# Optimization experiments

Measured on AMD Instinct MI355X. Metric: run time of the kernel, lower is better.

Reference implementation:

```python
import jax, jax.numpy as jnp
import numpy as np

STATE_LEN, SEQ_LEN, HIDDEN = 2048, 4096, 2048

def setup_inputs() -> dict:
    key = jax.random.key(0)
    k1, k2, k3, k4 = jax.random.split(key, 4)
    scale = 1.0 / np.sqrt(HIDDEN)
    return {
        "out_state": jax.random.normal(k1, (STATE_LEN, HIDDEN), dtype=jnp.float32),
        "history": jax.random.normal(k2, (SEQ_LEN, HIDDEN), dtype=jnp.float32),
        "W": jax.random.normal(k3, (HIDDEN, HIDDEN), dtype=jnp.float32) * scale,
        "b": jax.random.normal(k4, (HIDDEN,), dtype=jnp.float32) * scale,
    }

def reference(out_state, history, W, b):
    # method='general': energy_j = Linear(history_j) = history_j @ W.T + b
    # score[i, j] = out_state_i . energy_j  -> batched GEMM replacing the double loop
    energies = history @ W.T + b                 # [seq_len, hidden]
    scores = jnp.einsum('ih,jh->ij', out_state, energies)  # [state_len, seq_len]
    # F.softmax on a 2D tensor (legacy default) normalizes over dim=1 (rows)
    return jax.nn.softmax(scores, axis=-1)
```

## Files before the change

kernel.cpp:

```cpp
#include <hip/hip_runtime.h>


#define STATE_LEN 2048
#define SEQ_LEN   4096
#define HIDDEN    2048

#define BM 128
#define BN 128
#define BK 32

#define WAIT_VM8   0x0F78
#define WAIT_VM0   0x0F70
#define WAIT_LGKM0 0xC07F

typedef __bf16 bf16x8 __attribute__((ext_vector_type(8)));
typedef float f32x4 __attribute__((ext_vector_type(4)));

__device__ __forceinline__ unsigned short f32_to_bf16(float f) {
  unsigned u = __float_as_uint(f);
  u += 0x7FFFu + ((u >> 16) & 1u);
  return (unsigned short)(u >> 16);
}
__device__ __forceinline__ float bf16_to_f32(unsigned short h) {
  return __uint_as_float(((unsigned)h) << 16);
}

__device__ __forceinline__ void gld16(const void* g, void* l) {
  __builtin_amdgcn_global_load_lds(
      (const __attribute__((address_space(1))) unsigned int*)g,
      (__attribute__((address_space(3))) unsigned int*)l,
      16, 0, 0);
}

__global__ __launch_bounds__(256) void pack_all(
    const float* __restrict__ os, const float* __restrict__ hist,
    const float* __restrict__ W,
    unsigned short* __restrict__ ohi, unsigned short* __restrict__ olo,
    unsigned short* __restrict__ hhi, unsigned short* __restrict__ hlo,
    unsigned short* __restrict__ wthi, unsigned short* __restrict__ wtlo) {
  const int bx = blockIdx.x;
  const int t = threadIdx.x;
  if (bx < 12288) {
    const float* in;
    unsigned short *hi, *lo;
    int i;
    if (bx < 4096) {
      in = os; hi = ohi; lo = olo; i = (bx * 256 + t) * 4;
    } else {
      in = hist; hi = hhi; lo = hlo; i = ((bx - 4096) * 256 + t) * 4;
    }
    float4 v = *(const float4*)&in[i];
    ushort4 h, l;
    h.x = f32_to_bf16(v.x); l.x = f32_to_bf16(v.x - bf16_to_f32(h.x));
    h.y = f32_to_bf16(v.y); l.y = f32_to_bf16(v.y - bf16_to_f32(h.y));
    h.z = f32_to_bf16(v.z); l.z = f32_to_bf16(v.z - bf16_to_f32(h.z));
    h.w = f32_to_bf16(v.w); l.w = f32_to_bf16(v.w - bf16_to_f32(h.w));
    *(ushort4*)&hi[i] = h;
    *(ushort4*)&lo[i] = l;
  } else {
    __shared__ float tile[64][65];
    const int bt = bx - 12288;
    const int h0 = (bt & 31) * 64;
    const int k0 = (bt >> 5) * 64;
    const int lr = t >> 4;
    const int c4 = (t & 15) * 4;
#pragma unroll
    for (int pass = 0; pass < 4; ++pass) {
      const int row = pass * 16 + lr;
      float4 v = *(const float4*)&W[(size_t)(h0 + row) * HIDDEN + k0 + c4];
      tile[row][c4] = v.x; tile[row][c4 + 1] = v.y;
      tile[row][c4 + 2] = v.z; tile[row][c4 + 3] = v.w;
    }
    __syncthreads();
#pragma unroll
    for (int pass = 0; pass < 4; ++pass) {
      const int kl = pass * 16 + (t >> 4);
      const int hl = (t & 15) * 4;
      ushort4 h4, l4;
#pragma unroll
      for (int j = 0; j < 4; ++j) {
        const float x = tile[hl + j][kl];
        const unsigned short h = f32_to_bf16(x);
        ((unsigned short*)&h4)[j] = h;
        ((unsigned short*)&l4)[j] = f32_to_bf16(x - bf16_to_f32(h));
      }
      const size_t o = (size_t)(k0 + kl) * HIDDEN + h0 + hl;
      *(ushort4*)&wthi[o] = h4;
      *(ushort4*)&wtlo[o] = l4;
    }
  }
}

__global__ __launch_bounds__(256) void reduce_split2(
    const float* __restrict__ p0, const float* __restrict__ p1,
    unsigned short* __restrict__ hi, unsigned short* __restrict__ lo, int n) {
  int i = (blockIdx.x * 256 + threadIdx.x) * 4;
  if (i >= n) return;
  float4 a = *(const float4*)&p0[i];
  float4 b = *(const float4*)&p1[i];
  a.x += b.x; a.y += b.y; a.z += b.z; a.w += b.w;
  ushort4 h, l;
  h.x = f32_to_bf16(a.x); l.x = f32_to_bf16(a.x - bf16_to_f32(h.x));
  h.y = f32_to_bf16(a.y); l.y = f32_to_bf16(a.y - bf16_to_f32(h.y));
  h.z = f32_to_bf16(a.z); l.z = f32_to_bf16(a.z - bf16_to_f32(h.z));
  h.w = f32_to_bf16(a.w); l.w = f32_to_bf16(a.w - bf16_to_f32(h.w));
  *(ushort4*)&hi[i] = h;
  *(ushort4*)&lo[i] = l;
}

template <int KSPLIT>
__global__ __launch_bounds__(256, 2) void gemm_pipe(
    const unsigned short* __restrict__ Ahi, const unsigned short* __restrict__ Alo,
    const unsigned short* __restrict__ Bhi, const unsigned short* __restrict__ Blo,
    float* __restrict__ Cf0, float* __restrict__ Cf1, int M, int N, int K) {
  __shared__ __align__(16) unsigned short sA[2][2][BM * BK];
  __shared__ __align__(16) unsigned short sB[2][2][BN * BK];

  const int t = threadIdx.x;
  const int tileM = blockIdx.y * BM;
  const int tileN = blockIdx.x * BN;
  const int z = (KSPLIT > 1) ? blockIdx.z : 0;
  const int kBase = z * (K / KSPLIT);
  const int iters = (K / KSPLIT) / BK;
  float* Cf = (KSPLIT > 1 && z == 1) ? Cf1 : Cf0;

  const int rr = t >> 2;
  const int cc = t & 3;

  const int lane = t & 63;
  const int wave = t >> 6;
  const int wm = wave >> 1;
  const int wn = wave & 1;
  const int lr = lane & 15;
  const int kqc = lane >> 4;

  f32x4 acc[4][4] = {};

  auto stage = [&](int buf, int k0) {
#pragma unroll
    for (int p = 0; p < 2; ++p) {
      const int r = p * 64 + rr;
      const int q = cc ^ ((r >> 1) & 3);
      const size_t ga = (size_t)(tileM + r) * K + k0 + q * 8;
      const size_t gb = (size_t)(tileN + r) * K + k0 + q * 8;
      const int ls = r * BK + cc * 8;
      gld16(Ahi + ga, &sA[buf][0][ls]);
      gld16(Alo + ga, &sA[buf][1][ls]);
      gld16(Bhi + gb, &sB[buf][0][ls]);
      gld16(Blo + gb, &sB[buf][1][ls]);
    }
  };

  stage(0, kBase);

  for (int it = 0; it < iters; ++it) {
    const int buf = it & 1;
    if (it + 1 < iters) {
      stage(buf ^ 1, kBase + (it + 1) * BK);
      __builtin_amdgcn_s_waitcnt(WAIT_VM8);
    } else {
      __builtin_amdgcn_s_waitcnt(WAIT_VM0);
    }
    __builtin_amdgcn_s_barrier();

    bf16x8 ah[4], al[4], bh[4], bl[4];
#pragma unroll
    for (int mi = 0; mi < 4; ++mi) {
      const int R = wm * 64 + mi * 16 + lr;
      const int off = R * BK + (kqc ^ ((R >> 1) & 3)) * 8;
      ah[mi] = *(const bf16x8*)&sA[buf][0][off];
      al[mi] = *(const bf16x8*)&sA[buf][1][off];
    }
#pragma unroll
    for (int ni = 0; ni < 4; ++ni) {
      const int R = wn * 64 + ni * 16 + lr;
      const int off = R * BK + (kqc ^ ((R >> 1) & 3)) * 8;
      bh[ni] = *(const bf16x8*)&sB[buf][0][off];
      bl[ni] = *(const bf16x8*)&sB[buf][1][off];
    }
#pragma unroll
    for (int mi = 0; mi < 4; ++mi)
#pragma unroll
      for (int ni = 0; ni < 4; ++ni) {
        acc[mi][ni] = __builtin_amdgcn_mfma_f32_16x16x32_bf16(ah[mi], bh[ni], acc[mi][ni], 0, 0, 0);
        acc[mi][ni] = __builtin_amdgcn_mfma_f32_16x16x32_bf16(ah[mi], bl[ni], acc[mi][ni], 0, 0, 0);
        acc[mi][ni] = __builtin_amdgcn_mfma_f32_16x16x32_bf16(al[mi], bh[ni], acc[mi][ni], 0, 0, 0);
      }

    __builtin_amdgcn_s_waitcnt(WAIT_LGKM0);
    __builtin_amdgcn_s_barrier();
  }

#pragma unroll
  for (int mi = 0; mi < 4; ++mi)
#pragma unroll
    for (int ni = 0; ni < 4; ++ni)
#pragma unroll
      for (int e = 0; e < 4; ++e) {
        const int row = tileM + wm * 64 + mi * 16 + (lane >> 4) * 4 + e;
        const int col = tileN + wn * 64 + ni * 16 + lr;
        Cf[(size_t)row * N + col] = acc[mi][ni][e];
      }
}

__global__ __launch_bounds__(256) void softmax_rows(float* __restrict__ d, int cols) {
  const int row = blockIdx.x;
  float* p = d + (size_t)row * cols;
  const int t = threadIdx.x;
  const int lane = t & 63;
  const int wave = t >> 6;
  __shared__ float sred[4];

  float4 v[4];
  float m = -3.0e38f;
#pragma unroll
  for (int k = 0; k < 4; ++k) {
    v[k] = *(float4*)&p[(t + k * 256) * 4];
    m = fmaxf(m, fmaxf(fmaxf(v[k].x, v[k].y), fmaxf(v[k].z, v[k].w)));
  }
#pragma unroll
  for (int off = 32; off > 0; off >>= 1) m = fmaxf(m, __shfl_xor(m, off, 64));
  if (lane == 0) sred[wave] = m;
  __syncthreads();
  m = fmaxf(fmaxf(sred[0], sred[1]), fmaxf(sred[2], sred[3]));
  __syncthreads();

  float s = 0.f;
#pragma unroll
  for (int k = 0; k < 4; ++k) {
    v[k].x = __expf(v[k].x - m);
    v[k].y = __expf(v[k].y - m);
    v[k].z = __expf(v[k].z - m);
    v[k].w = __expf(v[k].w - m);
    s += (v[k].x + v[k].y) + (v[k].z + v[k].w);
  }
#pragma unroll
  for (int off = 32; off > 0; off >>= 1) s += __shfl_xor(s, off, 64);
  if (lane == 0) sred[wave] = s;
  __syncthreads();
  s = (sred[0] + sred[1]) + (sred[2] + sred[3]);
  const float inv = 1.0f / s;
#pragma unroll
  for (int k = 0; k < 4; ++k) {
    v[k].x *= inv; v[k].y *= inv; v[k].z *= inv; v[k].w *= inv;
    *(float4*)&p[(t + k * 256) * 4] = v[k];
  }
}

extern "C" void kernel_launch(void* const* d_in, const int* in_sizes, int n_in,
                              void* d_out, int out_size, void* d_ws, size_t ws_size,
                              hipStream_t stream) {
  const float* out_state = (const float*)d_in[0];
  const float* history   = (const float*)d_in[1];
  const float* W         = (const float*)d_in[2];
  float* out = (float*)d_out;

  char* ws = (char*)d_ws;
  const size_t MB = 1ull << 20;
  unsigned short* ohi  = (unsigned short*)(ws + 0 * MB);
  unsigned short* olo  = (unsigned short*)(ws + 8 * MB);
  unsigned short* wthi = (unsigned short*)(ws + 16 * MB);
  unsigned short* wtlo = (unsigned short*)(ws + 24 * MB);
  unsigned short* hhi  = (unsigned short*)(ws + 32 * MB);
  unsigned short* hlo  = (unsigned short*)(ws + 48 * MB);
  float*          pws  = (float*)(ws + 64 * MB);
  float* g1p0 = pws;
  float* g1p1 = pws + (size_t)STATE_LEN * HIDDEN;
  unsigned short* thi = (unsigned short*)(ws + 0 * MB);
  unsigned short* tlo = (unsigned short*)(ws + 8 * MB);

  pack_all<<<13312, 256, 0, stream>>>(out_state, history, W, ohi, olo, hhi, hlo,
                                      wthi, wtlo);
  gemm_pipe<2><<<dim3(HIDDEN / BN, STATE_LEN / BM, 2), 256, 0, stream>>>(
      ohi, olo, wthi, wtlo, g1p0, g1p1, STATE_LEN, HIDDEN, HIDDEN);
  reduce_split2<<<(STATE_LEN * HIDDEN) / 1024, 256, 0, stream>>>(
      g1p0, g1p1, thi, tlo, STATE_LEN * HIDDEN);
  gemm_pipe<1><<<dim3(SEQ_LEN / BN, STATE_LEN / BM, 1), 256, 0, stream>>>(
      thi, tlo, hhi, hlo, out, nullptr, STATE_LEN, SEQ_LEN, HIDDEN);
  softmax_rows<<<STATE_LEN, 256, 0, stream>>>(out, SEQ_LEN);
}
```

Baseline: 278.2 us.

## Use 256x256 GEMM tiles with deeper split-K and fuse partial sums into softmax

Both GEMMs move from 128x128 tiles with 256 threads to 256x256 tiles with 512 threads, raising operand reuse per LDS load. The first GEMM now uses 4-way split-K, with two of its partial buffers placed in the output buffer and summed in a 4-input reduce kernel. The second GEMM uses 2-way split-K so it fills the CUs with one wave of blocks, and its two partials are added inside the softmax kernel. The pack kernel also reorders its blocks so the W transpose blocks come first. The trade-offs are a 128KB LDS footprint per block, which limits occupancy to one block per CU, and an extra 32MB partial-sum read in the softmax.

Result: faster. 270.7 us (-2.7%).

```diff
diff --git a/kernel.cpp b/kernel.cpp
--- a/kernel.cpp
+++ b/kernel.cpp
@@ -5,8 +5,6 @@
 #define SEQ_LEN   4096
 #define HIDDEN    2048
 
-#define BM 128
-#define BN 128
 #define BK 32
 
 #define WAIT_VM8   0x0F78
@@ -40,14 +38,15 @@
     unsigned short* __restrict__ wthi, unsigned short* __restrict__ wtlo) {
   const int bx = blockIdx.x;
   const int t = threadIdx.x;
-  if (bx < 12288) {
+  if (bx >= 1024) {
+    const int b2 = bx - 1024;
     const float* in;
     unsigned short *hi, *lo;
     int i;
-    if (bx < 4096) {
-      in = os; hi = ohi; lo = olo; i = (bx * 256 + t) * 4;
+    if (b2 < 4096) {
+      in = os; hi = ohi; lo = olo; i = (b2 * 256 + t) * 4;
     } else {
-      in = hist; hi = hhi; lo = hlo; i = ((bx - 4096) * 256 + t) * 4;
+      in = hist; hi = hhi; lo = hlo; i = ((b2 - 4096) * 256 + t) * 4;
     }
     float4 v = *(const float4*)&in[i];
     ushort4 h, l;
@@ -59,7 +58,7 @@
     *(ushort4*)&lo[i] = l;
   } else {
     __shared__ float tile[64][65];
-    const int bt = bx - 12288;
+    const int bt = bx;
     const int h0 = (bt & 31) * 64;
     const int k0 = (bt >> 5) * 64;
     const int lr = t >> 4;
@@ -91,14 +90,20 @@
   }
 }
 
-__global__ __launch_bounds__(256) void reduce_split2(
+__global__ __launch_bounds__(256) void reduce_split4(
     const float* __restrict__ p0, const float* __restrict__ p1,
+    const float* __restrict__ p2, const float* __restrict__ p3,
     unsigned short* __restrict__ hi, unsigned short* __restrict__ lo, int n) {
   int i = (blockIdx.x * 256 + threadIdx.x) * 4;
   if (i >= n) return;
   float4 a = *(const float4*)&p0[i];
   float4 b = *(const float4*)&p1[i];
-  a.x += b.x; a.y += b.y; a.z += b.z; a.w += b.w;
+  float4 c = *(const float4*)&p2[i];
+  float4 d = *(const float4*)&p3[i];
+  a.x = (a.x + b.x) + (c.x + d.x);
+  a.y = (a.y + b.y) + (c.y + d.y);
+  a.z = (a.z + b.z) + (c.z + d.z);
+  a.w = (a.w + b.w) + (c.w + d.w);
   ushort4 h, l;
   h.x = f32_to_bf16(a.x); l.x = f32_to_bf16(a.x - bf16_to_f32(h.x));
   h.y = f32_to_bf16(a.y); l.y = f32_to_bf16(a.y - bf16_to_f32(h.y));
@@ -109,20 +114,22 @@
 }
 
 template <int KSPLIT>
-__global__ __launch_bounds__(256, 2) void gemm_pipe(
+__global__ __launch_bounds__(512, 2) void gemm_big(
     const unsigned short* __restrict__ Ahi, const unsigned short* __restrict__ Alo,
     const unsigned short* __restrict__ Bhi, const unsigned short* __restrict__ Blo,
-    float* __restrict__ Cf0, float* __restrict__ Cf1, int M, int N, int K) {
-  __shared__ __align__(16) unsigned short sA[2][2][BM * BK];
-  __shared__ __align__(16) unsigned short sB[2][2][BN * BK];
+    float* __restrict__ P0, float* __restrict__ P1,
+    float* __restrict__ P2, float* __restrict__ P3,
+    int M, int N, int K) {
+  __shared__ __align__(16) unsigned short sA[2][2][256 * BK];
+  __shared__ __align__(16) unsigned short sB[2][2][256 * BK];
 
   const int t = threadIdx.x;
-  const int tileM = blockIdx.y * BM;
-  const int tileN = blockIdx.x * BN;
+  const int tileM = blockIdx.y * 256;
+  const int tileN = blockIdx.x * 256;
   const int z = (KSPLIT > 1) ? blockIdx.z : 0;
   const int kBase = z * (K / KSPLIT);
   const int iters = (K / KSPLIT) / BK;
-  float* Cf = (KSPLIT > 1 && z == 1) ? Cf1 : Cf0;
+  float* Cf = (z == 0) ? P0 : (z == 1) ? P1 : (z == 2) ? P2 : P3;
 
   const int rr = t >> 2;
   const int cc = t & 3;
@@ -134,12 +141,12 @@
   const int lr = lane & 15;
   const int kqc = lane >> 4;
 
-  f32x4 acc[4][4] = {};
+  f32x4 acc[4][8] = {};
 
   auto stage = [&](int buf, int k0) {
 #pragma unroll
     for (int p = 0; p < 2; ++p) {
-      const int r = p * 64 + rr;
+      const int r = p * 128 + rr;
       const int q = cc ^ ((r >> 1) & 3);
       const size_t ga = (size_t)(tileM + r) * K + k0 + q * 8;
       const size_t gb = (size_t)(tileN + r) * K + k0 + q * 8;
@@ -163,7 +170,7 @@
     }
     __builtin_amdgcn_s_barrier();
 
-    bf16x8 ah[4], al[4], bh[4], bl[4];
+    bf16x8 ah[4], al[4];
 #pragma unroll
     for (int mi = 0; mi < 4; ++mi) {
       const int R = wm * 64 + mi * 16 + lr;
@@ -172,20 +179,26 @@
       al[mi] = *(const bf16x8*)&sA[buf][1][off];
     }
 #pragma unroll
-    for (int ni = 0; ni < 4; ++ni) {
-      const int R = wn * 64 + ni * 16 + lr;
-      const int off = R * BK + (kqc ^ ((R >> 1) & 3)) * 8;
-      bh[ni] = *(const bf16x8*)&sB[buf][0][off];
-      bl[ni] = *(const bf16x8*)&sB[buf][1][off];
-    }
-#pragma unroll
-    for (int mi = 0; mi < 4; ++mi)
-#pragma unroll
-      for (int ni = 0; ni < 4; ++ni) {
-        acc[mi][ni] = __builtin_amdgcn_mfma_f32_16x16x32_bf16(ah[mi], bh[ni], acc[mi][ni], 0, 0, 0);
-        acc[mi][ni] = __builtin_amdgcn_mfma_f32_16x16x32_bf16(ah[mi], bl[ni], acc[mi][ni], 0, 0, 0);
-        acc[mi][ni] = __builtin_amdgcn_mfma_f32_16x16x32_bf16(al[mi], bh[ni], acc[mi][ni], 0, 0, 0);
+    for (int nh = 0; nh < 2; ++nh) {
+      bf16x8 bh[4], bl[4];
+#pragma unroll
+      for (int nj = 0; nj < 4; ++nj) {
+        const int R = wn * 128 + (nh * 4 + nj) * 16 + lr;
+        const int off = R * BK + (kqc ^ ((R >> 1) & 3)) * 8;
+        bh[nj] = *(const bf16x8*)&sB[buf][0][off];
+        bl[nj] = *(const bf16x8*)&sB[buf][1][off];
       }
+#pragma unroll
+      for (int mi = 0; mi < 4; ++mi)
+#pragma unroll
+        for (int nj = 0; nj < 4; ++nj) {
+          f32x4 a = acc[mi][nh * 4 + nj];
+          a = __builtin_amdgcn_mfma_f32_16x16x32_bf16(ah[mi], bh[nj], a, 0, 0, 0);
+          a = __builtin_amdgcn_mfma_f32_16x16x32_bf16(ah[mi], bl[nj], a, 0, 0, 0);
+          a = __builtin_amdgcn_mfma_f32_16x16x32_bf16(al[mi], bh[nj], a, 0, 0, 0);
+          acc[mi][nh * 4 + nj] = a;
+        }
+    }
 
     __builtin_amdgcn_s_waitcnt(WAIT_LGKM0);
     __builtin_amdgcn_s_barrier();
@@ -194,18 +207,20 @@
 #pragma unroll
   for (int mi = 0; mi < 4; ++mi)
 #pragma unroll
-    for (int ni = 0; ni < 4; ++ni)
+    for (int ni = 0; ni < 8; ++ni)
 #pragma unroll
       for (int e = 0; e < 4; ++e) {
         const int row = tileM + wm * 64 + mi * 16 + (lane >> 4) * 4 + e;
-        const int col = tileN + wn * 64 + ni * 16 + lr;
+        const int col = tileN + wn * 128 + ni * 16 + lr;
         Cf[(size_t)row * N + col] = acc[mi][ni][e];
       }
 }
 
-__global__ __launch_bounds__(256) void softmax_rows(float* __restrict__ d, int cols) {
+__global__ __launch_bounds__(256) void softmax_rows2(
+    float* __restrict__ d, const float* __restrict__ p1, int cols) {
   const int row = blockIdx.x;
   float* p = d + (size_t)row * cols;
+  const float* q = p1 + (size_t)row * cols;
   const int t = threadIdx.x;
   const int lane = t & 63;
   const int wave = t >> 6;
@@ -215,8 +230,11 @@
   float m = -3.0e38f;
 #pragma unroll
   for (int k = 0; k < 4; ++k) {
-    v[k] = *(float4*)&p[(t + k * 256) * 4];
-    m = fmaxf(m, fmaxf(fmaxf(v[k].x, v[k].y), fmaxf(v[k].z, v[k].w)));
+    float4 a = *(const float4*)&p[(t + k * 256) * 4];
+    float4 b = *(const float4*)&q[(t + k * 256) * 4];
+    a.x += b.x; a.y += b.y; a.z += b.z; a.w += b.w;
+    v[k] = a;
+    m = fmaxf(m, fmaxf(fmaxf(a.x, a.y), fmaxf(a.z, a.w)));
   }
 #pragma unroll
   for (int off = 32; off > 0; off >>= 1) m = fmaxf(m, __shfl_xor(m, off, 64));
@@ -264,18 +282,22 @@
   unsigned short* hhi  = (unsigned short*)(ws + 32 * MB);
   unsigned short* hlo  = (unsigned short*)(ws + 48 * MB);
   float*          pws  = (float*)(ws + 64 * MB);
+
+  const size_t QSZ = (size_t)STATE_LEN * HIDDEN;
   float* g1p0 = pws;
-  float* g1p1 = pws + (size_t)STATE_LEN * HIDDEN;
+  float* g1p1 = pws + QSZ;
+  float* g1p2 = out;
+  float* g1p3 = out + QSZ;
   unsigned short* thi = (unsigned short*)(ws + 0 * MB);
   unsigned short* tlo = (unsigned short*)(ws + 8 * MB);
 
   pack_all<<<13312, 256, 0, stream>>>(out_state, history, W, ohi, olo, hhi, hlo,
                                       wthi, wtlo);
-  gemm_pipe<2><<<dim3(HIDDEN / BN, STATE_LEN / BM, 2), 256, 0, stream>>>(
-      ohi, olo, wthi, wtlo, g1p0, g1p1, STATE_LEN, HIDDEN, HIDDEN);
-  reduce_split2<<<(STATE_LEN * HIDDEN) / 1024, 256, 0, stream>>>(
-      g1p0, g1p1, thi, tlo, STATE_LEN * HIDDEN);
-  gemm_pipe<1><<<dim3(SEQ_LEN / BN, STATE_LEN / BM, 1), 256, 0, stream>>>(
-      thi, tlo, hhi, hlo, out, nullptr, STATE_LEN, SEQ_LEN, HIDDEN);
-  softmax_rows<<<STATE_LEN, 256, 0, stream>>>(out, SEQ_LEN);
-}
+  gemm_big<4><<<dim3(HIDDEN / 256, STATE_LEN / 256, 4), 512, 0, stream>>>(
+      ohi, olo, wthi, wtlo, g1p0, g1p1, g1p2, g1p3, STATE_LEN, HIDDEN, HIDDEN);
+  reduce_split4<<<(STATE_LEN * HIDDEN) / 1024, 256, 0, stream>>>(
+      g1p0, g1p1, g1p2, g1p3, thi, tlo, STATE_LEN * HIDDEN);
+  gemm_big<2><<<dim3(SEQ_LEN / 256, STATE_LEN / 256, 2), 512, 0, stream>>>(
+      thi, tlo, hhi, hlo, out, pws, nullptr, nullptr, STATE_LEN, SEQ_LEN, HIDDEN);
+  softmax_rows2<<<STATE_LEN, 256, 0, stream>>>(out, pws, SEQ_LEN);
+}
```
